# Kernel optimization log

Measured on AMD Instinct MI355X. Metric: run time of the kernel, lower is better.

Reference implementation:

```python
import jax, jax.numpy as jnp
import numpy as np

E, M, IN, OUT = 8, 8192, 2048, 8192


def setup_inputs() -> dict:
    key = jax.random.key(0)
    k1, k2, k3 = jax.random.split(key, 3)
    inputs = jax.random.normal(k1, (M, IN), dtype=jnp.float32)
    # truncated_normal(-3,3) scaled by init_scale/sqrt(In), matching MoELinear.init
    weight = jax.random.truncated_normal(k2, -3.0, 3.0, (E, IN, OUT), dtype=jnp.float32) * (1.0 / np.sqrt(IN))
    bias = jax.random.normal(k3, (OUT,), dtype=jnp.float32) * 0.02
    # tokens are pre-sorted by expert; balanced routing: M/E tokens per expert
    group_sizes = jnp.full((E,), M // E, dtype=jnp.int32)
    return {"inputs": inputs, "weight": weight, "group_sizes": group_sizes, "bias": bias}


def _ragged_matmul(inputs, weight, group_sizes):
    """Grouped GEMM: out[m] = inputs[m] @ weight[expert_of(m)].

    Tokens are contiguous per expert; group_sizes[e] gives the count for
    expert e. Same math as jax.lax.ragged_dot / megablox gmm.
    """
    n_experts = weight.shape[0]
    m = inputs.shape[0]
    # static-length repeat -> per-token expert id, jit-safe
    expert_ids = jnp.repeat(jnp.arange(n_experts, dtype=group_sizes.dtype),
                            group_sizes, total_repeat_length=m)  # [M]

    def body(acc, ew):
        e, w = ew  # w: [In, Out]
        mask = (expert_ids == e).astype(inputs.dtype)  # [M]
        return acc + (inputs * mask[:, None]) @ w, None

    acc0 = jnp.zeros((m, weight.shape[2]), dtype=inputs.dtype)
    out, _ = jax.lax.scan(body, acc0, (jnp.arange(n_experts, dtype=group_sizes.dtype), weight))
    return out


def reference(inputs, weight, group_sizes, bias):
    # MoELinear.__call__ (ragged_dot path): grouped matmul + bias
    return _ragged_matmul(inputs, weight, group_sizes) + bias
```

## Files before the change

kernel.cpp:

```cpp
#include <hip/hip_runtime.h>
#include <hip/hip_bf16.h>
#include <stdint.h>

#define E_ 8
#define M_ 8192
#define K_ 2048
#define N_ 8192

#define BM 256
#define BN 256
#define BK 64
#define NT (K_ / BK)
#define LDS_BYTES 131072

typedef __attribute__((ext_vector_type(8))) short bf16x8;
typedef __attribute__((ext_vector_type(4))) float f32x4;
typedef __attribute__((ext_vector_type(8))) unsigned short us8;

__device__ __forceinline__ unsigned short f2bf(float f) {
  union { float f; uint32_t u; } v; v.f = f;
  uint32_t u = v.u;
  uint32_t r = (u + 0x7FFFu + ((u >> 16) & 1u)) >> 16;
  return (unsigned short)r;
}

__device__ __forceinline__ unsigned short f2bf_hw(float f) {
  union { __hip_bfloat16 h; unsigned short u; } v;
  v.h = __float2bfloat16(f);
  return v.u;
}

__device__ __forceinline__ void gload_lds16(const void* g, void* l) {
  __builtin_amdgcn_global_load_lds(
      (const __attribute__((address_space(1))) unsigned int*)g,
      (__attribute__((address_space(3))) unsigned int*)l,
      16, 0, 0);
}

__global__ __launch_bounds__(256) void conv_a(const float* __restrict__ A,
                                              unsigned short* __restrict__ Ab,
                                              int n8) {
  int stride = gridDim.x * blockDim.x;
  for (int idx = blockIdx.x * blockDim.x + threadIdx.x; idx < n8; idx += stride) {
    const float4* p = reinterpret_cast<const float4*>(A) + (size_t)idx * 2;
    float4 x0 = p[0], x1 = p[1];
    us8 o;
    o[0] = f2bf(x0.x); o[1] = f2bf(x0.y); o[2] = f2bf(x0.z); o[3] = f2bf(x0.w);
    o[4] = f2bf(x1.x); o[5] = f2bf(x1.y); o[6] = f2bf(x1.z); o[7] = f2bf(x1.w);
    *reinterpret_cast<us8*>(Ab + (size_t)idx * 8) = o;
  }
}

__global__ __launch_bounds__(512, 2) void moe_gemm_fused(
    const unsigned short* __restrict__ Ab,
    const float* __restrict__ W,
    const int* __restrict__ gs,
    const float* __restrict__ bias,
    float* __restrict__ C) {
  extern __shared__ char smem[];

  int tile_n = blockIdx.x;
  int tile_m = blockIdx.y;

  int expert = -1, row_start = 0, rows = 0;
  {
    int acc = 0, off = 0;
    for (int e = 0; e < E_; ++e) {
      int g = gs[e];
      int t = (g + BM - 1) / BM;
      if (expert < 0 && tile_m < acc + t) {
        int lt = tile_m - acc;
        expert = e;
        row_start = off + lt * BM;
        rows = min(BM, g - lt * BM);
      }
      acc += t;
      off += g;
    }
    if (expert < 0) return;
  }

  const float* WfE = W + (size_t)expert * K_ * N_;

  int tid = threadIdx.x;
  int lane = tid & 63;
  int wave = tid >> 6;
  int wr = wave >> 2;
  int wc = wave & 3;
  int bh = wc >> 1;
  int ln15 = lane & 15;
  int n0 = tile_n * BN;

  int slot0 = (((lane >> 4) ^ ((ln15 >> 1) & 7)) << 4);
  int aBase = wr * 16384 + ln15 * 128;
  int bBase = 32768 + bh * 16384 + (wc & 1) * 8192 + ln15 * 128;

  int soff = tid * 16;
  int crow = tid >> 3;
  int lslot = (tid & 7) ^ ((crow >> 1) & 7);
  int scolA = lslot * 8;
  const unsigned short* aS[4];
  #pragma unroll
  for (int c = 0; c < 4; ++c) {
    int r = c * 64 + crow;
    int gr = r < rows ? r : 0;
    aS[c] = Ab + (size_t)(row_start + gr) * K_ + scolA;
  }
#define STG_A(DB, c, kt) \
  gload_lds16(aS[c] + (kt) * 64, smem + (DB) + (c) * 8192 + soff)

  int nB = (tid & 127) * 2;
  int kb0 = tid >> 7;
  const float* wB = WfE + (size_t)(n0 + nB);
  int sB0 = (kb0 ^ ((nB >> 1) & 7)) << 4;
  int sB1 = ((kb0 + 4) ^ ((nB >> 1) & 7)) << 4;
  int bw00 = 32768 + nB * 128 + sB0;
  int bw01 = 32768 + (nB + 1) * 128 + sB0;
  int bw10 = 32768 + nB * 128 + sB1;
  int bw11 = 32768 + (nB + 1) * 128 + sB1;

  float2 fSA0[8], fSA1[8], fSB0[8], fSB1[8];

#define LOAD_B(arr, KB, KT)                                                   \
  _Pragma("unroll") for (int j = 0; j < 8; ++j)                               \
    arr[j] = *(const float2*)(wB + (size_t)((KT) * 64 + (KB) * 8 + j) * N_);

#define CVT_WRITE(arr, WE, WO, DBN)                                           \
  do {                                                                        \
    us8 oe, oo;                                                               \
    _Pragma("unroll") for (int p = 0; p < 8; ++p) {                           \
      oe[p] = f2bf_hw(arr[p].x);                                              \
      oo[p] = f2bf_hw(arr[p].y);                                              \
    }                                                                         \
    *(us8*)(smem + (DBN) + (WE)) = oe;                                        \
    *(us8*)(smem + (DBN) + (WO)) = oo;                                        \
  } while (0)

  f32x4 acc4[8][4];
  #pragma unroll
  for (int i = 0; i < 8; ++i)
    #pragma unroll
    for (int j = 0; j < 4; ++j)
      acc4[i][j] = f32x4{0.f, 0.f, 0.f, 0.f};

#define DS_A(frag, DB, MH, KS)                                                \
  _Pragma("unroll") for (int mi = 0; mi < 4; ++mi)                            \
    frag[mi] = *(const bf16x8*)(smem + (DB) + aBase + (MH) * 8192 +           \
                                mi * 2048 + (slot0 ^ ((KS) << 6)));
#define DS_B(frag, DB, KS)                                                    \
  _Pragma("unroll") for (int nj = 0; nj < 4; ++nj)                            \
    frag[nj] = *(const bf16x8*)(smem + (DB) + bBase + nj * 2048 +             \
                                (slot0 ^ ((KS) << 6)));
#define MFMA16(MB, af, bf)                                                    \
  __builtin_amdgcn_s_setprio(1);                                              \
  _Pragma("unroll") for (int mi = 0; mi < 4; ++mi)                            \
    _Pragma("unroll") for (int nj = 0; nj < 4; ++nj)                          \
      acc4[(MB) + mi][nj] = __builtin_amdgcn_mfma_f32_16x16x32_bf16(          \
          af[mi], bf[nj], acc4[(MB) + mi][nj], 0, 0, 0);                      \
  __builtin_amdgcn_s_setprio(0);

#define TILE4(DB, DBN, W0, W1, L0, L1, KTA, KTB)                              \
  do {                                                                        \
    bf16x8 af[4], bf[4];                                                      \
                                                             \
    DS_A(af, DB, 0, 0); DS_B(bf, DB, 0);                                      \
    STG_A(DBN, 0, KTA); STG_A(DBN, 1, KTA);                                   \
    STG_A(DBN, 2, KTA); STG_A(DBN, 3, KTA);                                   \
    __builtin_amdgcn_sched_barrier(0);   \
    LOAD_B(L0, kb0, KTB);                                                     \
    __builtin_amdgcn_sched_barrier(0);                                        \
    __builtin_amdgcn_s_barrier();                                             \
    asm volatile("s_waitcnt lgkmcnt(0)" ::: "memory");                        \
    __builtin_amdgcn_sched_barrier(0);                                        \
    MFMA16(0, af, bf);                                                        \
    __builtin_amdgcn_s_barrier();                                             \
                                     \
    DS_A(af, DB, 1, 0);                                                       \
    LOAD_B(L1, kb0 + 4, KTB);                                                 \
    __builtin_amdgcn_sched_barrier(0);                                        \
    __builtin_amdgcn_s_barrier();                                             \
    asm volatile("s_waitcnt lgkmcnt(0)" ::: "memory");                        \
    __builtin_amdgcn_sched_barrier(0);                                        \
    MFMA16(4, af, bf);                                                        \
    __builtin_amdgcn_s_barrier();                                             \
                                           \
    DS_A(af, DB, 0, 1); DS_B(bf, DB, 1);                                      \
    CVT_WRITE(W0, bw00, bw01, DBN);                                           \
    __builtin_amdgcn_s_barrier();                                             \
    asm volatile("s_waitcnt lgkmcnt(0)" ::: "memory");                        \
    __builtin_amdgcn_sched_barrier(0);                                        \
    MFMA16(0, af, bf);                                                        \
    __builtin_amdgcn_s_barrier();                                             \
                                           \
    DS_A(af, DB, 1, 1);                                                       \
    CVT_WRITE(W1, bw10, bw11, DBN);                                           \
    __builtin_amdgcn_s_barrier();                                             \
    asm volatile("s_waitcnt lgkmcnt(0)" ::: "memory");                        \
    __builtin_amdgcn_sched_barrier(0);                                        \
    MFMA16(4, af, bf);                                                        \
    asm volatile("s_waitcnt vmcnt(16)" ::: "memory");  \
    __builtin_amdgcn_s_barrier();                                             \
  } while (0)

  STG_A(0, 0, 0); STG_A(0, 1, 0); STG_A(0, 2, 0); STG_A(0, 3, 0);
  __builtin_amdgcn_sched_barrier(0);
  LOAD_B(fSB0, kb0, 0); LOAD_B(fSB1, kb0 + 4, 0);
  __builtin_amdgcn_sched_barrier(0);
  CVT_WRITE(fSB0, bw00, bw01, 0);
  CVT_WRITE(fSB1, bw10, bw11, 0);
  LOAD_B(fSA0, kb0, 1); LOAD_B(fSA1, kb0 + 4, 1);
  __builtin_amdgcn_sched_barrier(0);
  asm volatile("s_waitcnt lgkmcnt(0)" ::: "memory");
  __builtin_amdgcn_s_barrier();

  for (int t2 = 0; t2 < NT; t2 += 2) {
    int ka0 = t2 + 1;
    int kb0t = (t2 + 2 >= NT) ? 0 : t2 + 2;
    int ka1 = kb0t;
    int kb1t = (t2 + 3 >= NT) ? 0 : t2 + 3;
    TILE4(0, 65536, fSA0, fSA1, fSB0, fSB1, ka0, kb0t);
    TILE4(65536, 0, fSB0, fSB1, fSA0, fSA1, ka1, kb1t);
  }
#undef TILE4
#undef DS_A
#undef DS_B
#undef MFMA16
#undef STG_A
#undef LOAD_B
#undef CVT_WRITE

  asm volatile("s_waitcnt vmcnt(0)" ::: "memory");

  float bv[4];
  #pragma unroll
  for (int nj = 0; nj < 4; ++nj) bv[nj] = bias[n0 + wc * 64 + nj * 16 + ln15];
  #pragma unroll
  for (int mi = 0; mi < 8; ++mi) {
    int r0 = wr * 128 + mi * 16 + (lane >> 4) * 4;
    #pragma unroll
    for (int r = 0; r < 4; ++r) {
      int lr = r0 + r;
      if (lr < rows) {
        float* Cp = C + (size_t)(row_start + lr) * N_ + n0 + wc * 64 + ln15;
        #pragma unroll
        for (int nj = 0; nj < 4; ++nj) Cp[nj * 16] = acc4[mi][nj][r] + bv[nj];
      }
    }
  }
}

__global__ __launch_bounds__(256) void moe_naive(const float* __restrict__ A,
                                                 const float* __restrict__ W,
                                                 const int* __restrict__ gs,
                                                 const float* __restrict__ bias,
                                                 float* __restrict__ C) {
  int col = blockIdx.x * 16 + (threadIdx.x & 15);
  int row = blockIdx.y * 16 + (threadIdx.x >> 4);
  int acc = 0, e = E_ - 1;
  for (int i = 0; i < E_; ++i) {
    int g = gs[i];
    if (row >= acc && row < acc + g) { e = i; break; }
    acc += g;
  }
  const float* a = A + (size_t)row * K_;
  const float* w = W + (size_t)e * K_ * N_ + col;
  float s = 0.f;
  for (int k = 0; k < K_; ++k) s += a[k] * w[(size_t)k * N_];
  C[(size_t)row * N_ + col] = s + bias[col];
}

extern "C" void kernel_launch(void* const* d_in, const int* in_sizes, int n_in,
                              void* d_out, int out_size, void* d_ws, size_t ws_size,
                              hipStream_t stream) {
  const float* A = (const float*)d_in[0];
  const float* W = (const float*)d_in[1];
  const int* gs = (const int*)d_in[2];
  const float* bias = (const float*)d_in[3];
  float* C = (float*)d_out;

  const size_t needA = (size_t)M_ * K_ * 2;

  (void)hipFuncSetAttribute((const void*)moe_gemm_fused,
                            hipFuncAttributeMaxDynamicSharedMemorySize, LDS_BYTES);

  if (ws_size >= needA) {
    unsigned short* Abf = (unsigned short*)d_ws;
    conv_a<<<2048, 256, 0, stream>>>(A, Abf, (M_ * K_) / 8);
    dim3 gg(N_ / BN, M_ / BM + E_);
    moe_gemm_fused<<<gg, 512, LDS_BYTES, stream>>>(Abf, W, gs, bias, C);
  } else {
    dim3 gn(N_ / 16, M_ / 16);
    moe_naive<<<gn, 256, 0, stream>>>(A, W, gs, bias, C);
  }
}
```

Before: 499.2 us.

## Shrink M tile to 128 rows and restructure pipeline into two-phase stages

Halves the M tile from 256 to 128 rows, so each wave holds a 64x64 accumulator tile instead of 128x64, and LDS per buffer drops to 48KB. The K-step pipeline is reorganised from four MFMA phases into two, with the B fp32-to-bf16 convert-and-write folded into each phase, and the LDS swizzle pattern changes. The aim is to cut register and LDS pressure so more blocks fit per CU and the tail is better balanced. The cost is lower arithmetic intensity: each fp32 weight tile is loaded and converted twice as often, which raises global traffic for W.

New measurement: 585.6 us. 1.17x slower.

```diff
diff --git a/kernel.cpp b/kernel.cpp
--- a/kernel.cpp
+++ b/kernel.cpp
@@ -7,11 +7,12 @@
 #define K_ 2048
 #define N_ 8192
 
-#define BM 256
+#define BM 128
 #define BN 256
 #define BK 64
 #define NT (K_ / BK)
-#define LDS_BYTES 131072
+#define TILE_B 49152
+#define LDS_BYTES 98304
 
 typedef __attribute__((ext_vector_type(8))) short bf16x8;
 typedef __attribute__((ext_vector_type(4))) float f32x4;
@@ -87,21 +88,20 @@
   int wave = tid >> 6;
   int wr = wave >> 2;
   int wc = wave & 3;
-  int bh = wc >> 1;
   int ln15 = lane & 15;
   int n0 = tile_n * BN;
 
-  int slot0 = (((lane >> 4) ^ ((ln15 >> 1) & 7)) << 4);
-  int aBase = wr * 16384 + ln15 * 128;
-  int bBase = 32768 + bh * 16384 + (wc & 1) * 8192 + ln15 * 128;
+  int slot0 = (((lane >> 4) ^ (ln15 & 7)) << 4);
+  int aBase = wr * 8192 + ln15 * 128;
+  int bBase = 16384 + wc * 8192 + ln15 * 128;
 
   int soff = tid * 16;
   int crow = tid >> 3;
-  int lslot = (tid & 7) ^ ((crow >> 1) & 7);
+  int lslot = (tid & 7) ^ (crow & 7);
   int scolA = lslot * 8;
-  const unsigned short* aS[4];
-  #pragma unroll
-  for (int c = 0; c < 4; ++c) {
+  const unsigned short* aS[2];
+  #pragma unroll
+  for (int c = 0; c < 2; ++c) {
     int r = c * 64 + crow;
     int gr = r < rows ? r : 0;
     aS[c] = Ab + (size_t)(row_start + gr) * K_ + scolA;
@@ -112,14 +112,12 @@
   int nB = (tid & 127) * 2;
   int kb0 = tid >> 7;
   const float* wB = WfE + (size_t)(n0 + nB);
-  int sB0 = (kb0 ^ ((nB >> 1) & 7)) << 4;
-  int sB1 = ((kb0 + 4) ^ ((nB >> 1) & 7)) << 4;
-  int bw00 = 32768 + nB * 128 + sB0;
-  int bw01 = 32768 + (nB + 1) * 128 + sB0;
-  int bw10 = 32768 + nB * 128 + sB1;
-  int bw11 = 32768 + (nB + 1) * 128 + sB1;
-
-  float2 fSA0[8], fSA1[8], fSB0[8], fSB1[8];
+  int bwE0 = 16384 + nB * 128 + ((kb0 ^ (nB & 7)) << 4);
+  int bwO0 = 16384 + (nB + 1) * 128 + ((kb0 ^ ((nB + 1) & 7)) << 4);
+  int bwE1 = 16384 + nB * 128 + (((kb0 + 4) ^ (nB & 7)) << 4);
+  int bwO1 = 16384 + (nB + 1) * 128 + (((kb0 + 4) ^ ((nB + 1) & 7)) << 4);
+
+  float2 sP0[8], sP1[8], sQ0[8], sQ1[8];
 
 #define LOAD_B(arr, KB, KT)                                                   \
   _Pragma("unroll") for (int j = 0; j < 8; ++j)                               \
@@ -136,92 +134,73 @@
     *(us8*)(smem + (DBN) + (WO)) = oo;                                        \
   } while (0)
 
-  f32x4 acc4[8][4];
-  #pragma unroll
-  for (int i = 0; i < 8; ++i)
+  f32x4 acc4[4][4];
+  #pragma unroll
+  for (int i = 0; i < 4; ++i)
     #pragma unroll
     for (int j = 0; j < 4; ++j)
       acc4[i][j] = f32x4{0.f, 0.f, 0.f, 0.f};
 
-#define DS_A(frag, DB, MH, KS)                                                \
+#define DS_A(frag, DB, KS)                                                    \
   _Pragma("unroll") for (int mi = 0; mi < 4; ++mi)                            \
-    frag[mi] = *(const bf16x8*)(smem + (DB) + aBase + (MH) * 8192 +           \
-                                mi * 2048 + (slot0 ^ ((KS) << 6)));
+    frag[mi] = *(const bf16x8*)(smem + (DB) + aBase + mi * 2048 +             \
+                                (slot0 ^ ((KS) << 6)));
 #define DS_B(frag, DB, KS)                                                    \
   _Pragma("unroll") for (int nj = 0; nj < 4; ++nj)                            \
     frag[nj] = *(const bf16x8*)(smem + (DB) + bBase + nj * 2048 +             \
                                 (slot0 ^ ((KS) << 6)));
-#define MFMA16(MB, af, bf)                                                    \
+#define MFMA16(af, bf)                                                        \
   __builtin_amdgcn_s_setprio(1);                                              \
   _Pragma("unroll") for (int mi = 0; mi < 4; ++mi)                            \
     _Pragma("unroll") for (int nj = 0; nj < 4; ++nj)                          \
-      acc4[(MB) + mi][nj] = __builtin_amdgcn_mfma_f32_16x16x32_bf16(          \
-          af[mi], bf[nj], acc4[(MB) + mi][nj], 0, 0, 0);                      \
+      acc4[mi][nj] = __builtin_amdgcn_mfma_f32_16x16x32_bf16(                 \
+          af[mi], bf[nj], acc4[mi][nj], 0, 0, 0);                             \
   __builtin_amdgcn_s_setprio(0);
 
-#define TILE4(DB, DBN, W0, W1, L0, L1, KTA, KTB)                              \
+#define TILE2(DB, DBN, Wr0, Wr1, L0, L1, KTA, KTB)                            \
   do {                                                                        \
     bf16x8 af[4], bf[4];                                                      \
-                                                             \
-    DS_A(af, DB, 0, 0); DS_B(bf, DB, 0);                                      \
+                                                                 \
+    DS_A(af, DB, 0); DS_B(bf, DB, 0);                                         \
     STG_A(DBN, 0, KTA); STG_A(DBN, 1, KTA);                                   \
-    STG_A(DBN, 2, KTA); STG_A(DBN, 3, KTA);                                   \
-    __builtin_amdgcn_sched_barrier(0);   \
     LOAD_B(L0, kb0, KTB);                                                     \
+    CVT_WRITE(Wr0, bwE0, bwO0, DBN);                                          \
     __builtin_amdgcn_sched_barrier(0);                                        \
     __builtin_amdgcn_s_barrier();                                             \
     asm volatile("s_waitcnt lgkmcnt(0)" ::: "memory");                        \
     __builtin_amdgcn_sched_barrier(0);                                        \
-    MFMA16(0, af, bf);                                                        \
-    __builtin_amdgcn_s_barrier();                                             \
-                                     \
-    DS_A(af, DB, 1, 0);                                                       \
+    MFMA16(af, bf);                                                           \
+    __builtin_amdgcn_s_barrier();                                             \
+                                                                 \
+    DS_A(af, DB, 1); DS_B(bf, DB, 1);                                         \
     LOAD_B(L1, kb0 + 4, KTB);                                                 \
+    CVT_WRITE(Wr1, bwE1, bwO1, DBN);                                          \
     __builtin_amdgcn_sched_barrier(0);                                        \
     __builtin_amdgcn_s_barrier();                                             \
     asm volatile("s_waitcnt lgkmcnt(0)" ::: "memory");                        \
     __builtin_amdgcn_sched_barrier(0);                                        \
-    MFMA16(4, af, bf);                                                        \
-    __builtin_amdgcn_s_barrier();                                             \
-                                           \
-    DS_A(af, DB, 0, 1); DS_B(bf, DB, 1);                                      \
-    CVT_WRITE(W0, bw00, bw01, DBN);                                           \
-    __builtin_amdgcn_s_barrier();                                             \
-    asm volatile("s_waitcnt lgkmcnt(0)" ::: "memory");                        \
-    __builtin_amdgcn_sched_barrier(0);                                        \
-    MFMA16(0, af, bf);                                                        \
-    __builtin_amdgcn_s_barrier();                                             \
-                                           \
-    DS_A(af, DB, 1, 1);                                                       \
-    CVT_WRITE(W1, bw10, bw11, DBN);                                           \
-    __builtin_amdgcn_s_barrier();                                             \
-    asm volatile("s_waitcnt lgkmcnt(0)" ::: "memory");                        \
-    __builtin_amdgcn_sched_barrier(0);                                        \
-    MFMA16(4, af, bf);                                                        \
+    MFMA16(af, bf);                                                           \
     asm volatile("s_waitcnt vmcnt(16)" ::: "memory");  \
     __builtin_amdgcn_s_barrier();                                             \
   } while (0)
 
-  STG_A(0, 0, 0); STG_A(0, 1, 0); STG_A(0, 2, 0); STG_A(0, 3, 0);
+  STG_A(0, 0, 0); STG_A(0, 1, 0);
+  LOAD_B(sP0, kb0, 0); LOAD_B(sP1, kb0 + 4, 0);
   __builtin_amdgcn_sched_barrier(0);
-  LOAD_B(fSB0, kb0, 0); LOAD_B(fSB1, kb0 + 4, 0);
-  __builtin_amdgcn_sched_barrier(0);
-  CVT_WRITE(fSB0, bw00, bw01, 0);
-  CVT_WRITE(fSB1, bw10, bw11, 0);
-  LOAD_B(fSA0, kb0, 1); LOAD_B(fSA1, kb0 + 4, 1);
+  CVT_WRITE(sP0, bwE0, bwO0, 0);
+  CVT_WRITE(sP1, bwE1, bwO1, 0);
+  LOAD_B(sQ0, kb0, 1); LOAD_B(sQ1, kb0 + 4, 1);
   __builtin_amdgcn_sched_barrier(0);
   asm volatile("s_waitcnt lgkmcnt(0)" ::: "memory");
   __builtin_amdgcn_s_barrier();
 
   for (int t2 = 0; t2 < NT; t2 += 2) {
-    int ka0 = t2 + 1;
-    int kb0t = (t2 + 2 >= NT) ? 0 : t2 + 2;
-    int ka1 = kb0t;
-    int kb1t = (t2 + 3 >= NT) ? 0 : t2 + 3;
-    TILE4(0, 65536, fSA0, fSA1, fSB0, fSB1, ka0, kb0t);
-    TILE4(65536, 0, fSB0, fSB1, fSA0, fSA1, ka1, kb1t);
-  }
-#undef TILE4
+    int k2 = (t2 + 2 >= NT) ? 0 : t2 + 2;
+    int k3 = (t2 + 3 >= NT) ? 0 : t2 + 3;
+    TILE2(0, TILE_B, sQ0, sQ1, sP0, sP1, t2 + 1, k2);
+    TILE2(TILE_B, 0, sP0, sP1, sQ0, sQ1, k2, k3);
+  }
+#undef TILE2
 #undef DS_A
 #undef DS_B
 #undef MFMA16
@@ -235,8 +214,8 @@
   #pragma unroll
   for (int nj = 0; nj < 4; ++nj) bv[nj] = bias[n0 + wc * 64 + nj * 16 + ln15];
   #pragma unroll
-  for (int mi = 0; mi < 8; ++mi) {
-    int r0 = wr * 128 + mi * 16 + (lane >> 4) * 4;
+  for (int mi = 0; mi < 4; ++mi) {
+    int r0 = wr * 64 + mi * 16 + (lane >> 4) * 4;
     #pragma unroll
     for (int r = 0; r < 4; ++r) {
       int lr = r0 + r;
```
